# Kernel optimization log

Measured on AMD Instinct MI355X. Metric: run time of the kernel, lower is better.

Reference implementation:

```python
import jax, jax.numpy as jnp
import numpy as np

B, S, E, H = 4, 2048, 1024, 16
HD = E // H  # head dim = 64
EPS = 1e-5


def layernorm(x, g, b):
    mu = jnp.mean(x, axis=-1, keepdims=True)
    var = jnp.var(x, axis=-1, keepdims=True)
    return (x - mu) * jax.lax.rsqrt(var + EPS) * g + b


def setup_inputs() -> dict:
    key = jax.random.key(0)
    ks = jax.random.split(key, 10)
    std = 1.0 / np.sqrt(E)
    def lin(k):
        kw, kb = jax.random.split(k)
        return (jax.random.uniform(kw, (E, E), jnp.float32, -std, std),
                jax.random.uniform(kb, (E,), jnp.float32, -std, std))
    wq, bq = lin(ks[0]); wk, bk = lin(ks[1]); wv, bv = lin(ks[2]); wp, bp = lin(ks[3])
    ones = jnp.ones((E,), jnp.float32); zeros = jnp.zeros((E,), jnp.float32)
    x = jax.random.normal(ks[4], (B, S, E), jnp.float32)
    return {
        'x': x,
        'wq': wq, 'bq': bq, 'wk': wk, 'bk': bk, 'wv': wv, 'bv': bv, 'wp': wp, 'bp': bp,
        'g_q': ones, 'be_q': zeros, 'g_k': ones, 'be_k': zeros,
        'g_v': ones, 'be_v': zeros, 'g_p': ones, 'be_p': zeros,
    }


def reference(x, wq, bq, wk, bk, wv, bv, wp, bp,
              g_q, be_q, g_k, be_k, g_v, be_v, g_p, be_p):
    def heads(t):  # [B,S,E] -> [B,H,S,HD]
        return t.reshape(B, S, H, HD).transpose(0, 2, 1, 3)

    Q = heads(layernorm(x @ wq.T + bq, g_q, be_q))
    K = heads(layernorm(x @ wk.T + bk, g_k, be_k))
    V = heads(layernorm(x @ wv.T + bv, g_v, be_v))

    scores = jnp.einsum('bhqd,bhkd->bhqk', Q, K) * (HD ** -0.5)
    causal = jnp.tril(jnp.ones((S, S), bool))  # [S,S]
    scores = jnp.where(causal[None, None], scores, -jnp.inf)
    attn = jax.nn.softmax(scores, axis=-1)
    out = jnp.einsum('bhqk,bhkd->bhqd', attn, V)
    out = out.transpose(0, 2, 1, 3).reshape(B, S, E)
    out = layernorm(out @ wp.T + bp, g_p, be_p)
    return out, V
```

## Files before the change

### kernel.cpp

```cpp
#include <hip/hip_runtime.h>
#include <hip/hip_bf16.h>

typedef unsigned short u16;
typedef __attribute__((ext_vector_type(8))) short short8;
typedef __attribute__((ext_vector_type(4))) float f32x4;

__device__ __forceinline__ float b2f(u16 u){
    unsigned v = ((unsigned)u) << 16; float f; __builtin_memcpy(&f, &v, 4); return f;
}
__device__ __forceinline__ u16 f2b(float f){
    unsigned v; __builtin_memcpy(&v, &f, 4);
    v += 0x7fffu + ((v >> 16) & 1u);
    return (u16)(v >> 16);
}
__device__ __forceinline__ u16 f2b_fast(float f){
    unsigned v; __builtin_memcpy(&v, &f, 4);
    return (u16)((v + 0x8000u) >> 16);
}

__device__ __forceinline__ void gload16(const void* g, void* l){
    __builtin_amdgcn_global_load_lds((const __attribute__((address_space(1))) unsigned int*)g,
                                     (__attribute__((address_space(3))) unsigned int*)l, 16, 0, 0);
}

__device__ __forceinline__ int swz(int row, int col){
    return row * 64 + (col ^ ((row & 7) << 3));
}

__global__ void cvt_k(const float* __restrict__ src, u16* __restrict__ dst)
{
    const int i = (blockIdx.x * 256 + threadIdx.x) * 4;
    float4 v = *(const float4*)&src[i];
    ushort4 o;
    o.x = f2b(v.x); o.y = f2b(v.y); o.z = f2b(v.z); o.w = f2b(v.w);
    *(ushort4*)&dst[i] = o;
}

__global__ void cvt4_k(const float* __restrict__ s0, const float* __restrict__ s1,
                       const float* __restrict__ s2, const float* __restrict__ s3,
                       u16* __restrict__ dst)
{
    const float* src = (blockIdx.y == 0) ? s0 : (blockIdx.y == 1) ? s1 :
                       (blockIdx.y == 2) ? s2 : s3;
    const int i = (blockIdx.x * 256 + threadIdx.x) * 4;
    float4 v = *(const float4*)&src[i];
    ushort4 o;
    o.x = f2b(v.x); o.y = f2b(v.y); o.z = f2b(v.z); o.w = f2b(v.w);
    *(ushort4*)&dst[(size_t)blockIdx.y * 1048576 + i] = o;
}

__global__ __launch_bounds__(256, 2)
void gemm3_k(const u16* __restrict__ A, const u16* __restrict__ Wb,
             const float* __restrict__ b0, const float* __restrict__ b1,
             const float* __restrict__ b2,
             u16* __restrict__ C0, u16* __restrict__ C1, u16* __restrict__ C2)
{
    __shared__ u16 As[128 * 32];
    __shared__ u16 Bs[128 * 32];
    const int K = 1024, N = 1024;
    const int mat = blockIdx.y >> 3;
    const int n0  = (blockIdx.y & 7) * 128;
    const u16* W = Wb + ((size_t)mat << 20);
    const float* bias = (mat == 0) ? b0 : (mat == 1) ? b1 : b2;
    u16* C = (mat == 0) ? C0 : (mat == 1) ? C1 : C2;

    const int tid  = threadIdx.x;
    const int wave = tid >> 6, lane = tid & 63;
    const int lg = lane >> 4, lr = lane & 15;
    const int m0 = blockIdx.x * 128;
    const int wm = (wave >> 1) * 64, wn = (wave & 1) * 64;

    const u16* aG = A + (size_t)(m0 + (tid >> 2)) * K + (tid & 3) * 8;
    const u16* bG = W + (size_t)(n0 + (tid >> 2)) * K + (tid & 3) * 8;
    char* asBase = (char*)As + wave * 1024;
    char* bsBase = (char*)Bs + wave * 1024;
    const size_t rstep = (size_t)64 * K;

    f32x4 acc[4][4] = {};

    for (int kt = 0; kt < K; kt += 32) {
        gload16(aG + kt,         asBase);
        gload16(aG + kt + rstep, asBase + 4096);
        gload16(bG + kt,         bsBase);
        gload16(bG + kt + rstep, bsBase + 4096);
        __syncthreads();

        short8 a[4], b[4];
#pragma unroll
        for (int i = 0; i < 4; ++i) a[i] = *(const short8*)&As[(wm + i*16 + lr)*32 + lg*8];
#pragma unroll
        for (int j = 0; j < 4; ++j) b[j] = *(const short8*)&Bs[(wn + j*16 + lr)*32 + lg*8];
        __builtin_amdgcn_s_setprio(1);
#pragma unroll
        for (int i = 0; i < 4; ++i)
#pragma unroll
            for (int j = 0; j < 4; ++j)
                acc[i][j] = __builtin_amdgcn_mfma_f32_16x16x32_bf16(a[i], b[j], acc[i][j], 0, 0, 0);
        __builtin_amdgcn_s_setprio(0);
        __syncthreads();
    }

#pragma unroll
    for (int j = 0; j < 4; ++j) {
        const int cn = n0 + wn + j*16 + lr;
        const float bv = bias[cn];
#pragma unroll
        for (int i = 0; i < 4; ++i) {
            const int cm = m0 + wm + i*16 + lg*4;
#pragma unroll
            for (int r = 0; r < 4; ++r)
                C[(size_t)(cm + r) * N + cn] = f2b(acc[i][j][r] + bv);
        }
    }
}

__global__ __launch_bounds__(256, 2)
void gemm_k(const u16* __restrict__ A, const u16* __restrict__ W,
            const float* __restrict__ bias, u16* __restrict__ C,
            int M, int N, int K)
{
    __shared__ u16 As[128 * 32];
    __shared__ u16 Bs[128 * 32];
    const int tid  = threadIdx.x;
    const int wave = tid >> 6, lane = tid & 63;
    const int lg = lane >> 4, lr = lane & 15;
    const int m0 = blockIdx.x * 128, n0 = blockIdx.y * 128;
    const int wm = (wave >> 1) * 64, wn = (wave & 1) * 64;

    const u16* aG = A + (size_t)(m0 + (tid >> 2)) * K + (tid & 3) * 8;
    const u16* bG = W + (size_t)(n0 + (tid >> 2)) * K + (tid & 3) * 8;
    char* asBase = (char*)As + wave * 1024;
    char* bsBase = (char*)Bs + wave * 1024;
    const size_t rstep = (size_t)64 * K;

    f32x4 acc[4][4] = {};

    for (int kt = 0; kt < K; kt += 32) {
        gload16(aG + kt,         asBase);
        gload16(aG + kt + rstep, asBase + 4096);
        gload16(bG + kt,         bsBase);
        gload16(bG + kt + rstep, bsBase + 4096);
        __syncthreads();

        short8 a[4], b[4];
#pragma unroll
        for (int i = 0; i < 4; ++i) a[i] = *(const short8*)&As[(wm + i*16 + lr)*32 + lg*8];
#pragma unroll
        for (int j = 0; j < 4; ++j) b[j] = *(const short8*)&Bs[(wn + j*16 + lr)*32 + lg*8];
        __builtin_amdgcn_s_setprio(1);
#pragma unroll
        for (int i = 0; i < 4; ++i)
#pragma unroll
            for (int j = 0; j < 4; ++j)
                acc[i][j] = __builtin_amdgcn_mfma_f32_16x16x32_bf16(a[i], b[j], acc[i][j], 0, 0, 0);
        __builtin_amdgcn_s_setprio(0);
        __syncthreads();
    }

#pragma unroll
    for (int j = 0; j < 4; ++j) {
        const int cn = n0 + wn + j*16 + lr;
        const float bv = bias[cn];
#pragma unroll
        for (int i = 0; i < 4; ++i) {
            const int cm = m0 + wm + i*16 + lg*4;
#pragma unroll
            for (int r = 0; r < 4; ++r)
                C[(size_t)(cm + r) * N + cn] = f2b(acc[i][j][r] + bv);
        }
    }
}

__global__ void ln3_k(u16* D0, u16* D1, const u16* __restrict__ Sv,
                      const float* __restrict__ g_q, const float* __restrict__ be_q,
                      const float* __restrict__ g_k, const float* __restrict__ be_k,
                      const float* __restrict__ g_v, const float* __restrict__ be_v,
                      float* __restrict__ Vf)
{
    __shared__ float red[8];
    const int which = blockIdx.y;
    const u16* src = (which == 0) ? D0 : (which == 1) ? D1 : Sv;
    const float* g  = (which == 0) ? g_q  : (which == 1) ? g_k  : g_v;
    const float* be = (which == 0) ? be_q : (which == 1) ? be_k : be_v;
    const float scale = (which == 0) ? 0.125f * 1.4426950408889634f : 1.0f;

    const int row = blockIdx.x;
    const int tid = threadIdx.x;
    const int lane = tid & 63, wave = tid >> 6;
    ushort4 v = *(const ushort4*)&src[(size_t)row * 1024 + tid * 4];
    float f[4] = { b2f(v.x), b2f(v.y), b2f(v.z), b2f(v.w) };
    float s  = f[0] + f[1] + f[2] + f[3];
    float ss = f[0]*f[0] + f[1]*f[1] + f[2]*f[2] + f[3]*f[3];
#pragma unroll
    for (int off = 32; off; off >>= 1) { s += __shfl_down(s, off); ss += __shfl_down(ss, off); }
    if (lane == 0) { red[wave] = s; red[4 + wave] = ss; }
    __syncthreads();
    s  = red[0] + red[1] + red[2] + red[3];
    ss = red[4] + red[5] + red[6] + red[7];
    const float mean = s * (1.0f / 1024.0f);
    const float var  = fmaxf(ss * (1.0f / 1024.0f) - mean * mean, 0.0f);
    const float rs   = rsqrtf(var + 1e-5f);
    float o[4];
#pragma unroll
    for (int k = 0; k < 4; ++k) {
        const int e = tid * 4 + k;
        o[k] = ((f[k] - mean) * rs * g[e] + be[e]) * scale;
    }
    if (which == 2) {
        const int b = row >> 11, sIdx = row & 2047;
        const int h = tid >> 4, hd = (tid * 4) & 63;
        float4 ov = { o[0], o[1], o[2], o[3] };
        *(float4*)&Vf[(((size_t)(b * 16 + h) * 2048 + sIdx) << 6) + hd] = ov;
    } else {
        u16* dst = (which == 0) ? D0 : D1;
        ushort4 ov; ov.x = f2b(o[0]); ov.y = f2b(o[1]); ov.z = f2b(o[2]); ov.w = f2b(o[3]);
        *(ushort4*)&dst[(size_t)row * 1024 + tid * 4] = ov;
    }
}

__global__ void lnf_k(const u16* __restrict__ src, const float* __restrict__ g,
                      const float* __restrict__ be, float* __restrict__ dst)
{
    __shared__ float red[8];
    const int row = blockIdx.x;
    const int tid = threadIdx.x;
    const int lane = tid & 63, wave = tid >> 6;
    ushort4 v = *(const ushort4*)&src[(size_t)row * 1024 + tid * 4];
    float f[4] = { b2f(v.x), b2f(v.y), b2f(v.z), b2f(v.w) };
    float s  = f[0] + f[1] + f[2] + f[3];
    float ss = f[0]*f[0] + f[1]*f[1] + f[2]*f[2] + f[3]*f[3];
#pragma unroll
    for (int off = 32; off; off >>= 1) { s += __shfl_down(s, off); ss += __shfl_down(ss, off); }
    if (lane == 0) { red[wave] = s; red[4 + wave] = ss; }
    __syncthreads();
    s  = red[0] + red[1] + red[2] + red[3];
    ss = red[4] + red[5] + red[6] + red[7];
    const float mean = s * (1.0f / 1024.0f);
    const float var  = fmaxf(ss * (1.0f / 1024.0f) - mean * mean, 0.0f);
    const float rs   = rsqrtf(var + 1e-5f);
    float4 ov;
    ov.x = (f[0] - mean) * rs * g[tid*4+0] + be[tid*4+0];
    ov.y = (f[1] - mean) * rs * g[tid*4+1] + be[tid*4+1];
    ov.z = (f[2] - mean) * rs * g[tid*4+2] + be[tid*4+2];
    ov.w = (f[3] - mean) * rs * g[tid*4+3] + be[tid*4+3];
    *(float4*)&dst[(size_t)row * 1024 + tid * 4] = ov;
}

__global__ void vtr_k(const float* __restrict__ Vf, u16* __restrict__ Vt)
{
    __shared__ float T[64 * 65];
    const int bh = blockIdx.x >> 5, st = blockIdx.x & 31;
    const int tid = threadIdx.x;
    const float* src = Vf + (size_t)bh * 2048 * 64 + (size_t)st * 64 * 64;
#pragma unroll
    for (int it = 0; it < 4; ++it) {
        const int fid = tid + it * 256;
        const int r = fid >> 4, c4 = fid & 15;
        float4 v = *(const float4*)&src[r * 64 + c4 * 4];
        T[r * 65 + c4*4 + 0] = v.x;
        T[r * 65 + c4*4 + 1] = v.y;
        T[r * 65 + c4*4 + 2] = v.z;
        T[r * 65 + c4*4 + 3] = v.w;
    }
    __syncthreads();
    u16* dst = Vt + (size_t)bh * 64 * 2048 + (size_t)st * 64;
#pragma unroll
    for (int it = 0; it < 2; ++it) {
        const int oid = tid + it * 256;
        const int hd = oid >> 3, ch = oid & 7;
        u16 tmp[8];
#pragma unroll
        for (int j = 0; j < 8; ++j) tmp[j] = f2b(T[(ch * 8 + j) * 65 + hd]);
        const int base = 32 * (ch >> 2) + 4 * ((ch >> 1) & 1);
        const int p0 = base + 8 * ((2 * ch + 0) & 3);
        const int p1 = base + 8 * ((2 * ch + 1) & 3);
        ushort4 lo = { tmp[0], tmp[1], tmp[2], tmp[3] };
        ushort4 hi = { tmp[4], tmp[5], tmp[6], tmp[7] };
        *(ushort4*)&dst[(size_t)hd * 2048 + p0] = lo;
        *(ushort4*)&dst[(size_t)hd * 2048 + p1] = hi;
    }
}

__global__ __launch_bounds__(512, 4)
void attn_k(const u16* __restrict__ Qf, const u16* __restrict__ Kf,
            const u16* __restrict__ Vt, u16* __restrict__ O)
{
    __shared__ u16 Ks [2][64 * 64];
    __shared__ u16 Vts[2][64 * 64];
    const int lin = (int)blockIdx.x + (int)blockIdx.y * 16;
    const int xcd = lin & 7, idx = lin >> 3;
    const int bh  = xcd * 8 + (idx & 7);
    const int qt  = 15 - (idx >> 3);
    const int b = bh >> 4, h = bh & 15;
    const int tid = threadIdx.x, wave = tid >> 6, lane = tid & 63;
    const int lg = lane >> 4, lr = lane & 15;
    const u16* Qbh = Qf + ((size_t)b * 2048) * 1024 + h * 64;
    const u16* Kbh = Kf + ((size_t)b * 2048) * 1024 + h * 64;
    const u16* Vbh = Vt + (size_t)bh * 64 * 2048;
    u16* Obh = O + ((size_t)b * 2048) * 1024 + h * 64;

    const int q0w  = qt * 128 + wave * 16;
    const int qrow = q0w + lr;
    const short8 qf0 = *(const short8*)&Qbh[(size_t)qrow * 1024 + lg * 8];
    const short8 qf1 = *(const short8*)&Qbh[(size_t)qrow * 1024 + 32 + lg * 8];

    const int nkv = 2 * qt + 2;
    const int sr = tid >> 3;
    const int sc = (tid & 7) ^ (sr & 7);

    f32x4 oacc[4] = {};
    float l_r = 0.f, m_r = -1e30f;

    gload16(Kbh + (size_t)sr * 1024 + sc * 8, (char*)Ks[0]  + wave * 1024);
    gload16(Vbh + (size_t)sr * 2048 + sc * 8, (char*)Vts[0] + wave * 1024);
    __syncthreads();

    for (int kv = 0; kv < nkv; ++kv) {
        const int cur = kv & 1, nxt = cur ^ 1;
        const int kv0 = kv * 64;
        if (kv + 1 < nkv) {
            const int kvn = kv0 + 64;
            gload16(Kbh + (size_t)(kvn + sr) * 1024 + sc * 8, (char*)Ks[nxt]  + wave * 1024);
            gload16(Vbh + (size_t)sr * 2048 + kvn + sc * 8,   (char*)Vts[nxt] + wave * 1024);
        }

        if (kv0 <= q0w + 15) {
            f32x4 sacc[4];
#pragma unroll
            for (int c = 0; c < 4; ++c) {
                const int row = c * 16 + lr;
                const short8 k0 = *(const short8*)&Ks[cur][swz(row, lg * 8)];
                const short8 k1 = *(const short8*)&Ks[cur][swz(row, 32 + lg * 8)];
                f32x4 z = { 0.f, 0.f, 0.f, 0.f };
                __builtin_amdgcn_s_setprio(1);
                z = __builtin_amdgcn_mfma_f32_16x16x32_bf16(k0, qf0, z, 0, 0, 0);
                z = __builtin_amdgcn_mfma_f32_16x16x32_bf16(k1, qf1, z, 0, 0, 0);
                __builtin_amdgcn_s_setprio(0);
                sacc[c] = z;
            }

            if (kv0 + 63 > q0w) {
                const int kbase = kv0 + 4 * lg;
#pragma unroll
                for (int c = 0; c < 4; ++c)
#pragma unroll
                    for (int r = 0; r < 4; ++r)
                        if (kbase + c * 16 + r > qrow) sacc[c][r] = -1e30f;
            }

            float mx0 = fmaxf(fmaxf(sacc[0][0], sacc[0][1]), fmaxf(sacc[0][2], sacc[0][3]));
            float mx1 = fmaxf(fmaxf(sacc[1][0], sacc[1][1]), fmaxf(sacc[1][2], sacc[1][3]));
            float mx2 = fmaxf(fmaxf(sacc[2][0], sacc[2][1]), fmaxf(sacc[2][2], sacc[2][3]));
            float mx3 = fmaxf(fmaxf(sacc[3][0], sacc[3][1]), fmaxf(sacc[3][2], sacc[3][3]));
            float mx = fmaxf(fmaxf(mx0, mx1), fmaxf(mx2, mx3));
            mx = fmaxf(mx, __shfl_xor(mx, 16));
            mx = fmaxf(mx, __shfl_xor(mx, 32));

            const float df = mx - m_r;
            if (__any(df > 8.0f)) {
                const float mn = (df > 8.0f) ? mx : m_r;
                const float al = exp2f(m_r - mn);
                m_r = mn;
                l_r *= al;
#pragma unroll
                for (int r = 0; r < 4; ++r) {
                    const float alo = __shfl(al, 4 * lg + r);
#pragma unroll
                    for (int c2 = 0; c2 < 4; ++c2) oacc[c2][r] *= alo;
                }
            }

            float ts = 0.f;
#pragma unroll
            for (int c = 0; c < 4; ++c)
#pragma unroll
                for (int r = 0; r < 4; ++r) {
                    const float pv = exp2f(sacc[c][r] - m_r);
                    sacc[c][r] = pv;
                    ts += pv;
                }
            ts += __shfl_xor(ts, 16);
            ts += __shfl_xor(ts, 32);
            l_r += ts;

#pragma unroll
            for (int m2 = 0; m2 < 2; ++m2) {
                short8 pa;
#pragma unroll
                for (int r = 0; r < 4; ++r) {
                    pa[r]     = (short)f2b_fast(sacc[2 * m2][r]);
                    pa[4 + r] = (short)f2b_fast(sacc[2 * m2 + 1][r]);
                }
                __builtin_amdgcn_s_setprio(1);
#pragma unroll
                for (int c2 = 0; c2 < 4; ++c2) {
                    const short8 vb = *(const short8*)&Vts[cur][swz(c2 * 16 + lr, m2 * 32 + lg * 8)];
                    oacc[c2] = __builtin_amdgcn_mfma_f32_16x16x32_bf16(pa, vb, oacc[c2], 0, 0, 0);
                }
                __builtin_amdgcn_s_setprio(0);
            }
        }
        __syncthreads();
    }

    float lo[4];
#pragma unroll
    for (int r = 0; r < 4; ++r) lo[r] = 1.0f / __shfl(l_r, 4 * lg + r);
#pragma unroll
    for (int c2 = 0; c2 < 4; ++c2)
#pragma unroll
        for (int r = 0; r < 4; ++r) {
            const float ov = oacc[c2][r] * lo[r];
            Obh[(size_t)(q0w + 4 * lg + r) * 1024 + c2 * 16 + lr] = f2b(ov);
        }
}

extern "C" void kernel_launch(void* const* d_in, const int* in_sizes, int n_in,
                              void* d_out, int out_size, void* d_ws, size_t ws_size,
                              hipStream_t stream)
{
    (void)in_sizes; (void)n_in; (void)out_size; (void)ws_size;
    const float* x   = (const float*)d_in[0];
    const float* wq  = (const float*)d_in[1];  const float* bq   = (const float*)d_in[2];
    const float* wk  = (const float*)d_in[3];  const float* bk   = (const float*)d_in[4];
    const float* wv  = (const float*)d_in[5];  const float* bv   = (const float*)d_in[6];
    const float* wp  = (const float*)d_in[7];  const float* bp   = (const float*)d_in[8];
    const float* g_q = (const float*)d_in[9];  const float* be_q = (const float*)d_in[10];
    const float* g_k = (const float*)d_in[11]; const float* be_k = (const float*)d_in[12];
    const float* g_v = (const float*)d_in[13]; const float* be_v = (const float*)d_in[14];
    const float* g_p = (const float*)d_in[15]; const float* be_p = (const float*)d_in[16];

    float* outF = (float*)d_out;
    float* Vf   = outF + 8388608;
    u16* D0 = (u16*)d_out;
    u16* D1 = (u16*)d_out + 8388608;
    u16* xb = (u16*)d_out + 16777216;
    char* ws = (char*)d_ws;
    u16* S0  = (u16*)ws;
    u16* wb  = (u16*)(ws + 16777216);
    u16* wpb = wb + 3145728;

    const dim3 bb(256);
    cvt4_k<<<dim3(1024, 4), bb, 0, stream>>>(wq, wk, wv, wp, wb);
    cvt_k<<<dim3(8192), bb, 0, stream>>>(x, xb);

    gemm3_k<<<dim3(64, 24), bb, 0, stream>>>(xb, wb, bq, bk, bv, D0, D1, S0);
    ln3_k<<<dim3(8192, 3), bb, 0, stream>>>(D0, D1, S0, g_q, be_q, g_k, be_k, g_v, be_v, Vf);
    vtr_k<<<dim3(2048), bb, 0, stream>>>(Vf, S0);
    attn_k<<<dim3(16, 64), dim3(512), 0, stream>>>(D0, D1, S0, D0);
    gemm_k<<<dim3(64, 8), bb, 0, stream>>>(D0, wpb, bp, S0, 8192, 1024, 1024);
    lnf_k<<<dim3(8192), bb, 0, stream>>>(S0, g_p, be_p, outF);
}
```

Before: 214.9 us.

## Merge conversion kernels and streamline attention inner loop addressing and packing

Fuses the weight and input fp32-to-bf16 conversion kernels into one launch. In the attention kernel, the two shared buffers become a single flat LDS array with precomputed swizzled byte offsets and incrementing global pointers. The diagonal test becomes a block-index compare, and bf16 packing of probabilities uses a perm instruction that packs two values at once. The max and sum reductions are reshaped into shallower trees, aiming to cut per-iteration ALU and address arithmetic at the cost of extra register pressure.

```diff
diff --git a/kernel.cpp b/kernel.cpp
--- a/kernel.cpp
+++ b/kernel.cpp
@@ -13,9 +13,9 @@
     v += 0x7fffu + ((v >> 16) & 1u);
     return (u16)(v >> 16);
 }
-__device__ __forceinline__ u16 f2b_fast(float f){
-    unsigned v; __builtin_memcpy(&v, &f, 4);
-    return (u16)((v + 0x8000u) >> 16);
+__device__ __forceinline__ unsigned pk2(float lo, float hi){
+    unsigned a, b; __builtin_memcpy(&a, &lo, 4); __builtin_memcpy(&b, &hi, 4);
+    return __builtin_amdgcn_perm(b + 0x8000u, a + 0x8000u, 0x07060302u);
 }
 
 __device__ __forceinline__ void gload16(const void* g, void* l){
@@ -27,26 +27,25 @@
     return row * 64 + (col ^ ((row & 7) << 3));
 }
 
-__global__ void cvt_k(const float* __restrict__ src, u16* __restrict__ dst)
-{
-    const int i = (blockIdx.x * 256 + threadIdx.x) * 4;
+__global__ void cvtall_k(const float* __restrict__ x,
+                         const float* __restrict__ wq, const float* __restrict__ wk,
+                         const float* __restrict__ wv, const float* __restrict__ wp,
+                         u16* __restrict__ xb, u16* __restrict__ wb)
+{
+    const int blk = blockIdx.x;
+    const float* src; u16* dst;
+    if (blk < 8192) {
+        src = x + (size_t)blk * 1024; dst = xb + (size_t)blk * 1024;
+    } else {
+        const int m = (blk - 8192) >> 10, r = (blk - 8192) & 1023;
+        const float* w = (m == 0) ? wq : (m == 1) ? wk : (m == 2) ? wv : wp;
+        src = w + (size_t)r * 1024; dst = wb + ((size_t)m << 20) + (size_t)r * 1024;
+    }
+    const int i = threadIdx.x * 4;
     float4 v = *(const float4*)&src[i];
     ushort4 o;
     o.x = f2b(v.x); o.y = f2b(v.y); o.z = f2b(v.z); o.w = f2b(v.w);
     *(ushort4*)&dst[i] = o;
-}
-
-__global__ void cvt4_k(const float* __restrict__ s0, const float* __restrict__ s1,
-                       const float* __restrict__ s2, const float* __restrict__ s3,
-                       u16* __restrict__ dst)
-{
-    const float* src = (blockIdx.y == 0) ? s0 : (blockIdx.y == 1) ? s1 :
-                       (blockIdx.y == 2) ? s2 : s3;
-    const int i = (blockIdx.x * 256 + threadIdx.x) * 4;
-    float4 v = *(const float4*)&src[i];
-    ushort4 o;
-    o.x = f2b(v.x); o.y = f2b(v.y); o.z = f2b(v.z); o.w = f2b(v.w);
-    *(ushort4*)&dst[(size_t)blockIdx.y * 1048576 + i] = o;
 }
 
 __global__ __launch_bounds__(256, 2)
@@ -285,8 +284,7 @@
 void attn_k(const u16* __restrict__ Qf, const u16* __restrict__ Kf,
             const u16* __restrict__ Vt, u16* __restrict__ O)
 {
-    __shared__ u16 Ks [2][64 * 64];
-    __shared__ u16 Vts[2][64 * 64];
+    __shared__ u16 Lds[16384];
     const int lin = (int)blockIdx.x + (int)blockIdx.y * 16;
     const int xcd = lin & 7, idx = lin >> 3;
     const int bh  = xcd * 8 + (idx & 7);
@@ -304,33 +302,46 @@
     const short8 qf0 = *(const short8*)&Qbh[(size_t)qrow * 1024 + lg * 8];
     const short8 qf1 = *(const short8*)&Qbh[(size_t)qrow * 1024 + 32 + lg * 8];
 
-    const int nkv = 2 * qt + 2;
+    const int nkv    = 2 * qt + 2;
+    const int diagkv = q0w >> 6;
+
+    const int kro0 = swz(lr, lg * 8) * 2;
+    const int kro1 = swz(lr, 32 + lg * 8) * 2;
+    const int vro0 = 8192 + kro0;
+    const int vro1 = 8192 + kro1;
+    const char* ldsB = (const char*)Lds;
+
     const int sr = tid >> 3;
-    const int sc = (tid & 7) ^ (sr & 7);
+    const int sc8 = ((tid & 7) ^ (sr & 7)) * 8;
+    const u16* kg = Kbh + (size_t)sr * 1024 + sc8;
+    const u16* vg = Vbh + (size_t)sr * 2048 + sc8;
+    const int stKo = wave * 1024;
 
     f32x4 oacc[4] = {};
     float l_r = 0.f, m_r = -1e30f;
 
-    gload16(Kbh + (size_t)sr * 1024 + sc * 8, (char*)Ks[0]  + wave * 1024);
-    gload16(Vbh + (size_t)sr * 2048 + sc * 8, (char*)Vts[0] + wave * 1024);
+    gload16(kg, (char*)Lds + stKo);
+    gload16(vg, (char*)Lds + 8192 + stKo);
+    kg += 65536; vg += 64;
     __syncthreads();
 
+    int rbuf = 0, sbuf = 16384;
     for (int kv = 0; kv < nkv; ++kv) {
-        const int cur = kv & 1, nxt = cur ^ 1;
-        const int kv0 = kv * 64;
         if (kv + 1 < nkv) {
-            const int kvn = kv0 + 64;
-            gload16(Kbh + (size_t)(kvn + sr) * 1024 + sc * 8, (char*)Ks[nxt]  + wave * 1024);
-            gload16(Vbh + (size_t)sr * 2048 + kvn + sc * 8,   (char*)Vts[nxt] + wave * 1024);
+            gload16(kg, (char*)Lds + sbuf + stKo);
+            gload16(vg, (char*)Lds + sbuf + 8192 + stKo);
+            kg += 65536; vg += 64;
         }
 
-        if (kv0 <= q0w + 15) {
+        if (kv <= diagkv) {
+            const char* kp0 = ldsB + (rbuf + kro0);
+            const char* kp1 = ldsB + (rbuf + kro1);
+
             f32x4 sacc[4];
 #pragma unroll
             for (int c = 0; c < 4; ++c) {
-                const int row = c * 16 + lr;
-                const short8 k0 = *(const short8*)&Ks[cur][swz(row, lg * 8)];
-                const short8 k1 = *(const short8*)&Ks[cur][swz(row, 32 + lg * 8)];
+                const short8 k0 = *(const short8*)(kp0 + c * 2048);
+                const short8 k1 = *(const short8*)(kp1 + c * 2048);
                 f32x4 z = { 0.f, 0.f, 0.f, 0.f };
                 __builtin_amdgcn_s_setprio(1);
                 z = __builtin_amdgcn_mfma_f32_16x16x32_bf16(k0, qf0, z, 0, 0, 0);
@@ -339,8 +350,8 @@
                 sacc[c] = z;
             }
 
-            if (kv0 + 63 > q0w) {
-                const int kbase = kv0 + 4 * lg;
+            if (kv == diagkv) {
+                const int kbase = kv * 64 + 4 * lg;
 #pragma unroll
                 for (int c = 0; c < 4; ++c)
 #pragma unroll
@@ -348,11 +359,13 @@
                         if (kbase + c * 16 + r > qrow) sacc[c][r] = -1e30f;
             }
 
-            float mx0 = fmaxf(fmaxf(sacc[0][0], sacc[0][1]), fmaxf(sacc[0][2], sacc[0][3]));
-            float mx1 = fmaxf(fmaxf(sacc[1][0], sacc[1][1]), fmaxf(sacc[1][2], sacc[1][3]));
-            float mx2 = fmaxf(fmaxf(sacc[2][0], sacc[2][1]), fmaxf(sacc[2][2], sacc[2][3]));
-            float mx3 = fmaxf(fmaxf(sacc[3][0], sacc[3][1]), fmaxf(sacc[3][2], sacc[3][3]));
-            float mx = fmaxf(fmaxf(mx0, mx1), fmaxf(mx2, mx3));
+            float t0 = fmaxf(fmaxf(sacc[0][0], sacc[0][1]), sacc[0][2]);
+            float t1 = fmaxf(fmaxf(sacc[0][3], sacc[1][0]), sacc[1][1]);
+            float t2 = fmaxf(fmaxf(sacc[1][2], sacc[1][3]), sacc[2][0]);
+            float t3 = fmaxf(fmaxf(sacc[2][1], sacc[2][2]), sacc[2][3]);
+            float t4 = fmaxf(fmaxf(sacc[3][0], sacc[3][1]), sacc[3][2]);
+            float mx = fmaxf(fmaxf(fmaxf(t0, t1), fmaxf(t2, t3)),
+                             fmaxf(t4, sacc[3][3]));
             mx = fmaxf(mx, __shfl_xor(mx, 16));
             mx = fmaxf(mx, __shfl_xor(mx, 32));
 
@@ -370,36 +383,41 @@
                 }
             }
 
-            float ts = 0.f;
 #pragma unroll
             for (int c = 0; c < 4; ++c)
 #pragma unroll
-                for (int r = 0; r < 4; ++r) {
-                    const float pv = exp2f(sacc[c][r] - m_r);
-                    sacc[c][r] = pv;
-                    ts += pv;
-                }
-            ts += __shfl_xor(ts, 16);
-            ts += __shfl_xor(ts, 32);
-            l_r += ts;
-
+                for (int r = 0; r < 4; ++r) sacc[c][r] = exp2f(sacc[c][r] - m_r);
+            {
+                float s0 = (sacc[0][0] + sacc[0][1]) + (sacc[0][2] + sacc[0][3]);
+                float s1 = (sacc[1][0] + sacc[1][1]) + (sacc[1][2] + sacc[1][3]);
+                float s2 = (sacc[2][0] + sacc[2][1]) + (sacc[2][2] + sacc[2][3]);
+                float s3 = (sacc[3][0] + sacc[3][1]) + (sacc[3][2] + sacc[3][3]);
+                float ts = (s0 + s1) + (s2 + s3);
+                ts += __shfl_xor(ts, 16);
+                ts += __shfl_xor(ts, 32);
+                l_r += ts;
+            }
+
+            const char* vp0 = ldsB + (rbuf + vro0);
+            const char* vp1 = ldsB + (rbuf + vro1);
 #pragma unroll
             for (int m2 = 0; m2 < 2; ++m2) {
-                short8 pa;
-#pragma unroll
-                for (int r = 0; r < 4; ++r) {
-                    pa[r]     = (short)f2b_fast(sacc[2 * m2][r]);
-                    pa[4 + r] = (short)f2b_fast(sacc[2 * m2 + 1][r]);
-                }
+                union { unsigned w[4]; short8 v; } pa;
+                pa.w[0] = pk2(sacc[2*m2][0],   sacc[2*m2][1]);
+                pa.w[1] = pk2(sacc[2*m2][2],   sacc[2*m2][3]);
+                pa.w[2] = pk2(sacc[2*m2+1][0], sacc[2*m2+1][1]);
+                pa.w[3] = pk2(sacc[2*m2+1][2], sacc[2*m2+1][3]);
+                const char* vp = m2 ? vp1 : vp0;
                 __builtin_amdgcn_s_setprio(1);
 #pragma unroll
                 for (int c2 = 0; c2 < 4; ++c2) {
-                    const short8 vb = *(const short8*)&Vts[cur][swz(c2 * 16 + lr, m2 * 32 + lg * 8)];
-                    oacc[c2] = __builtin_amdgcn_mfma_f32_16x16x32_bf16(pa, vb, oacc[c2], 0, 0, 0);
+                    const short8 vb = *(const short8*)(vp + c2 * 2048);
+                    oacc[c2] = __builtin_amdgcn_mfma_f32_16x16x32_bf16(pa.v, vb, oacc[c2], 0, 0, 0);
                 }
                 __builtin_amdgcn_s_setprio(0);
             }
         }
+        rbuf ^= 16384; sbuf ^= 16384;
         __syncthreads();
     }
 
@@ -441,8 +459,7 @@
     u16* wpb = wb + 3145728;
 
     const dim3 bb(256);
-    cvt4_k<<<dim3(1024, 4), bb, 0, stream>>>(wq, wk, wv, wp, wb);
-    cvt_k<<<dim3(8192), bb, 0, stream>>>(x, xb);
+    cvtall_k<<<dim3(12288), bb, 0, stream>>>(x, wq, wk, wv, wp, xb, wb);
 
     gemm3_k<<<dim3(64, 24), bb, 0, stream>>>(xb, wb, bq, bk, bv, D0, D1, S0);
     ln3_k<<<dim3(8192, 3), bb, 0, stream>>>(D0, D1, S0, g_q, be_q, g_k, be_k, g_v, be_v, Vf);
```

After: 208.9 us. -2.8%, faster.
